# Optimization experiments

Measured on AMD Instinct MI355X. Metric: run time of the kernel, lower is better.

Reference implementation:

```python
import jax, jax.numpy as jnp
import numpy as np
from jax import lax

B, S, N, F = 64, 512, 30, 1
H, HD = 2, 8              # n_heads, head_dim (gat_hidden=16)
GH = H * HD               # gat_hidden
P = 64                    # projection_dim
LH = 64                   # lstm_hidden
ALPHA = 0.2


def setup_inputs() -> dict:
    key = jax.random.key(0)
    ks = jax.random.split(key, 16)
    x = jax.random.normal(ks[0], (B, S, N, F), dtype=jnp.float32)
    adj = jax.random.randint(ks[1], (N, N), 0, 2).astype(jnp.float32)
    adj = jnp.maximum(adj, jnp.eye(N, dtype=jnp.float32))  # self-loops, no empty rows
    sc = 0.1
    W_gat = sc * jax.random.normal(ks[2], (H, F, HD), dtype=jnp.float32)
    a_src = sc * jax.random.normal(ks[3], (H, HD), dtype=jnp.float32)
    a_dst = sc * jax.random.normal(ks[4], (H, HD), dtype=jnp.float32)
    W_proj = sc * jax.random.normal(ks[5], (N * GH, P), dtype=jnp.float32)
    b_proj = jnp.zeros((P,), dtype=jnp.float32)
    W_ih0 = sc * jax.random.normal(ks[6], (4 * LH, P), dtype=jnp.float32)
    W_hh0 = sc * jax.random.normal(ks[7], (4 * LH, LH), dtype=jnp.float32)
    b_ih0 = jnp.zeros((4 * LH,), dtype=jnp.float32)
    b_hh0 = jnp.zeros((4 * LH,), dtype=jnp.float32)
    W_ih1 = sc * jax.random.normal(ks[8], (4 * LH, LH), dtype=jnp.float32)
    W_hh1 = sc * jax.random.normal(ks[9], (4 * LH, LH), dtype=jnp.float32)
    b_ih1 = jnp.zeros((4 * LH,), dtype=jnp.float32)
    b_hh1 = jnp.zeros((4 * LH,), dtype=jnp.float32)
    W_out = sc * jax.random.normal(ks[10], (LH, N * F), dtype=jnp.float32)
    b_out = jnp.zeros((N * F,), dtype=jnp.float32)
    return dict(x=x, adj=adj, W_gat=W_gat, a_src=a_src, a_dst=a_dst,
                W_proj=W_proj, b_proj=b_proj,
                W_ih0=W_ih0, W_hh0=W_hh0, b_ih0=b_ih0, b_hh0=b_hh0,
                W_ih1=W_ih1, W_hh1=W_hh1, b_ih1=b_ih1, b_hh1=b_hh1,
                W_out=W_out, b_out=b_out)


def _gat(x_flat, adj, W_gat, a_src, a_dst):
    # x_flat: (BS, N, F)
    h = jnp.einsum('bnf,hfd->bhnd', x_flat, W_gat)          # (BS, H, N, HD)
    e_src = jnp.einsum('bhnd,hd->bhn', h, a_src)
    e_dst = jnp.einsum('bhnd,hd->bhn', h, a_dst)
    e = e_src[..., :, None] + e_dst[..., None, :]           # (BS, H, N, N)
    e = jnp.where(e >= 0, e, ALPHA * e)                     # leaky_relu
    e = jnp.where(adj == 0, -jnp.inf, e)
    attn = jax.nn.softmax(e, axis=-1)
    attn = jnp.nan_to_num(attn, nan=0.0)
    out = jnp.einsum('bhij,bhjd->bhid', attn, h)            # (BS, H, N, HD)
    out = jnp.swapaxes(out, 1, 2).reshape(out.shape[0], N, GH)  # head-concat
    out = jnp.where(out > 0, out, jnp.expm1(out))           # elu
    attn_avg = attn.mean(axis=1)                            # (BS, N, N)
    return out, attn_avg


def _lstm_layer(xs, W_ih, W_hh, b_ih, b_hh):
    # xs: (B, S, D) -> (B, S, LH); torch gate order i,f,g,o
    b = xs.shape[0]
    h0 = jnp.zeros((b, LH), xs.dtype)
    c0 = jnp.zeros((b, LH), xs.dtype)

    def step(carry, x_t):
        h, c = carry
        gates = x_t @ W_ih.T + b_ih + h @ W_hh.T + b_hh
        i, f, g, o = jnp.split(gates, 4, axis=-1)
        i, f, o = jax.nn.sigmoid(i), jax.nn.sigmoid(f), jax.nn.sigmoid(o)
        g = jnp.tanh(g)
        c = f * c + i * g
        h = o * jnp.tanh(c)
        return (h, c), h

    (_, _), hs = lax.scan(step, (h0, c0), jnp.swapaxes(xs, 0, 1))
    return jnp.swapaxes(hs, 0, 1)


def reference(x, adj, W_gat, a_src, a_dst, W_proj, b_proj,
              W_ih0, W_hh0, b_ih0, b_hh0, W_ih1, W_hh1, b_ih1, b_hh1,
              W_out, b_out):
    b, s, n, f = x.shape
    x_flat = x.reshape(b * s, n, f)
    gat_out, attn = _gat(x_flat, adj, W_gat, a_src, a_dst)   # (BS,N,GH),(BS,N,N)
    gat_seq = gat_out.reshape(b, s, n * GH)
    gat_seq = jax.nn.relu(gat_seq @ W_proj + b_proj)         # (B,S,P)
    h1 = _lstm_layer(gat_seq, W_ih0, W_hh0, b_ih0, b_hh0)
    h2 = _lstm_layer(h1, W_ih1, W_hh1, b_ih1, b_hh1)
    recon = h2 @ W_out + b_out                               # (B,S,N*F)
    attn_last = attn.reshape(b, s, n, n)[:, -1]              # (B,N,N)
    return recon, attn_last
```

## Files before the change

kernel.cpp:

```cpp
#include <hip/hip_runtime.h>
#include <math.h>

#define BS_TOT 32768
#define NN 30
#define HHD 8
#define GHH 16
#define LHH 64
#define SSS 512
#define BBB 64
#define RECON_SIZE (BBB*SSS*NN)

__device__ __forceinline__ float fsigmoid(float x) {
    return 1.f / (1.f + __expf(-x));
}
__device__ __forceinline__ float ftanh(float x) {
    float ax = fabsf(x);
    float e = __expf(-2.f * ax);
    float r = (1.f - e) / (1.f + e);
    return copysignf(r, x);
}

#define NB 16
__global__ __launch_bounds__(256) void gat_proj_kernel(
    const float* __restrict__ x, const float* __restrict__ adj,
    const float* __restrict__ W_gat, const float* __restrict__ a_src,
    const float* __restrict__ a_dst, const float* __restrict__ W_proj,
    const float* __restrict__ b_proj, float* __restrict__ gat_seq,
    float* __restrict__ attn_out)
{
    __shared__ __align__(16) float gat[NB][480];
    __shared__ __align__(16) float wchunk[96*64];
    __shared__ float x_s[NB][32];
    __shared__ unsigned adjbits[32];

    const int t = threadIdx.x;
    const int bs_base = blockIdx.x * NB;

    for (int rep = 0; rep < 2; ++rep) {
        int idx = rep*256 + t;
        int bl = idx >> 5, j = idx & 31;
        if (j < NN) x_s[bl][j] = x[(bs_base + bl)*NN + j];
    }
    if (t < NN) {
        unsigned bits = 0;
        for (int j = 0; j < NN; ++j)
            if (adj[t*NN + j] != 0.0f) bits |= (1u << j);
        adjbits[t] = bits;
    }
    __syncthreads();

    const int wave = t >> 6, lane = t & 63;
    const int h = lane >> 5, i = lane & 31;
    const bool act = (i < NN);

    float wg[HHD];
    float s_h = 0.f, t_h = 0.f;
    #pragma unroll
    for (int d = 0; d < HHD; ++d) {
        float w = W_gat[h*HHD + d];
        wg[d] = w;
        s_h += w * a_src[h*HHD + d];
        t_h += w * a_dst[h*HHD + d];
    }

    for (int r = 0; r < 4; ++r) {
        const int bl = wave*4 + r;
        const int bs = bs_base + bl;
        const unsigned bits = act ? adjbits[i & 31] : 0u;
        const float xi = act ? x_s[bl][i] : 0.f;
        const float esrc = xi * s_h;

        float m = -1e30f;
        for (int j = 0; j < NN; ++j) {
            if (bits & (1u << j)) {
                float e = esrc + x_s[bl][j] * t_h;
                e = (e >= 0.f) ? e : 0.2f * e;
                m = fmaxf(m, e);
            }
        }
        float Z = 0.f, Sx = 0.f;
        for (int j = 0; j < NN; ++j) {
            if (bits & (1u << j)) {
                float e = esrc + x_s[bl][j] * t_h;
                e = (e >= 0.f) ? e : 0.2f * e;
                float p = expf(e - m);
                Z += p;
                Sx += p * x_s[bl][j];
            }
        }
        const float wsum = Sx / Z;

        if (act) {
            float tmp[8];
            #pragma unroll
            for (int d = 0; d < 8; ++d) {
                float v = wsum * wg[d];
                tmp[d] = (v > 0.f) ? v : expm1f(v);
            }
            float4 v0 = make_float4(tmp[0], tmp[1], tmp[2], tmp[3]);
            float4 v1 = make_float4(tmp[4], tmp[5], tmp[6], tmp[7]);
            *(float4*)&gat[bl][i*GHH + h*HHD]     = v0;
            *(float4*)&gat[bl][i*GHH + h*HHD + 4] = v1;
        }

        if ((bs & (SSS-1)) == (SSS-1)) {
            const int b = bs >> 9;
            for (int j = 0; j < NN; ++j) {
                float a = 0.f;
                if (bits & (1u << j)) {
                    float e = esrc + x_s[bl][j] * t_h;
                    e = (e >= 0.f) ? e : 0.2f * e;
                    a = expf(e - m) / Z;
                }
                float ao = __shfl_xor(a, 32, 64);
                if (act && h == 0)
                    attn_out[b*(NN*NN) + i*NN + j] = 0.5f * (a + ao);
            }
        }
    }
    __syncthreads();

    const int p = t & 63, grp = t >> 6;
    float acc0 = 0.f, acc1 = 0.f, acc2 = 0.f, acc3 = 0.f;
    for (int c = 0; c < 5; ++c) {
        #pragma unroll
        for (int rep = 0; rep < 24; ++rep)
            wchunk[rep*256 + t] = W_proj[c*6144 + rep*256 + t];
        __syncthreads();
        for (int kk = 0; kk < 96; kk += 4) {
            float4 g0 = *(const float4*)&gat[grp*4 + 0][c*96 + kk];
            float4 g1 = *(const float4*)&gat[grp*4 + 1][c*96 + kk];
            float4 g2 = *(const float4*)&gat[grp*4 + 2][c*96 + kk];
            float4 g3 = *(const float4*)&gat[grp*4 + 3][c*96 + kk];
            float w0 = wchunk[(kk+0)*64 + p];
            float w1 = wchunk[(kk+1)*64 + p];
            float w2 = wchunk[(kk+2)*64 + p];
            float w3 = wchunk[(kk+3)*64 + p];
            acc0 += g0.x*w0 + g0.y*w1 + g0.z*w2 + g0.w*w3;
            acc1 += g1.x*w0 + g1.y*w1 + g1.z*w2 + g1.w*w3;
            acc2 += g2.x*w0 + g2.y*w1 + g2.z*w2 + g2.w*w3;
            acc3 += g3.x*w0 + g3.y*w1 + g3.z*w2 + g3.w*w3;
        }
        __syncthreads();
    }
    const float bp = b_proj[p];
    gat_seq[(bs_base + grp*4 + 0)*64 + p] = fmaxf(acc0 + bp, 0.f);
    gat_seq[(bs_base + grp*4 + 1)*64 + p] = fmaxf(acc1 + bp, 0.f);
    gat_seq[(bs_base + grp*4 + 2)*64 + p] = fmaxf(acc2 + bp, 0.f);
    gat_seq[(bs_base + grp*4 + 3)*64 + p] = fmaxf(acc3 + bp, 0.f);
}

__global__ __launch_bounds__(256) void xproj_kernel(
    const float* __restrict__ xin,
    const float* __restrict__ W,
    const float* __restrict__ b_ih, const float* __restrict__ b_hh,
    float* __restrict__ gx)
{
    __shared__ __align__(16) float xt[64][64];
    const int t = threadIdx.x;
    const int r0 = blockIdx.x * 64;

    for (int i = t; i < 64*16; i += 256) {
        int r = i >> 4, c4 = (i & 15) << 2;
        *(float4*)&xt[r][c4] = *(const float4*)&xin[(size_t)(r0 + r)*64 + c4];
    }
    float4 w[16];
    #pragma unroll
    for (int i = 0; i < 16; ++i) w[i] = *(const float4*)&W[t*64 + 4*i];
    const float bias = b_ih[t] + b_hh[t];
    __syncthreads();

    for (int r = 0; r < 64; ++r) {
        float a0 = 0.f, a1 = 0.f, a2 = 0.f, a3 = 0.f;
        #pragma unroll
        for (int i = 0; i < 16; ++i) {
            float4 v = *(const float4*)&xt[r][4*i];
            a0 = fmaf(v.x, w[i].x, a0); a1 = fmaf(v.y, w[i].y, a1);
            a2 = fmaf(v.z, w[i].z, a2); a3 = fmaf(v.w, w[i].w, a3);
        }
        gx[(size_t)(r0 + r)*256 + t] = bias + ((a0 + a1) + (a2 + a3));
    }
}

__global__ __launch_bounds__(256) void lstm_rec_kernel(
    const float* __restrict__ gx,
    const float* __restrict__ W_hh,
    float* __restrict__ h_out)
{
    __shared__ __align__(16) float whh[256][68];
    __shared__ float h_s[64];
    __shared__ float gates[256];

    const int t = threadIdx.x;
    const int b = blockIdx.x;

    for (int i = t; i < 256*16; i += 256) {
        int r = i >> 4, c4 = (i & 15) << 2;
        *(float4*)&whh[r][c4] = *(const float4*)&W_hh[r*64 + c4];
    }
    if (t < 64) h_s[t] = 0.f;
    __syncthreads();

    const float* __restrict__ gxb = gx + (size_t)b * SSS * 256;
    float* __restrict__ hrow = h_out + (size_t)b * SSS * 64;

    float c = 0.f;
    float gx_cur = gxb[t];
    const int sect = t >> 6;

    for (int tt = 0; tt < SSS; ++tt) {
        float gx_next = (tt + 1 < SSS) ? gxb[(size_t)(tt+1)*256 + t] : 0.f;

        float a0 = 0.f, a1 = 0.f, a2 = 0.f, a3 = 0.f;
        #pragma unroll
        for (int i = 0; i < 16; ++i) {
            float4 h4 = *(const float4*)&h_s[4*i];
            float4 w4 = *(const float4*)&whh[t][4*i];
            a0 = fmaf(h4.x, w4.x, a0); a1 = fmaf(h4.y, w4.y, a1);
            a2 = fmaf(h4.z, w4.z, a2); a3 = fmaf(h4.w, w4.w, a3);
        }
        const float acc = gx_cur + ((a0 + a1) + (a2 + a3));
        const float a = (sect == 2) ? ftanh(acc) : fsigmoid(acc);
        gates[t] = a;
        __syncthreads();

        if (t < 64) {
            float ig = gates[t], fg = gates[64+t], gg = gates[128+t], og = gates[192+t];
            c = fg*c + ig*gg;
            float hv = og * ftanh(c);
            h_s[t] = hv;
            hrow[(size_t)tt*64 + t] = hv;
        }
        gx_cur = gx_next;
        __syncthreads();
    }
}

__global__ __launch_bounds__(256) void recon_kernel(
    const float* __restrict__ h2, const float* __restrict__ W_out,
    const float* __restrict__ b_out, float* __restrict__ out)
{
    __shared__ __align__(16) float hl[8*64];
    const int t = threadIdx.x;
    const int bs_base = blockIdx.x * 8;

    hl[t]       = h2[(size_t)bs_base*64 + t];
    hl[256 + t] = h2[(size_t)bs_base*64 + 256 + t];
    __syncthreads();

    if (t < 240) {
        const int bl = t / 30;
        const int n  = t - bl*30;
        float acc = b_out[n];
        #pragma unroll
        for (int k = 0; k < 64; ++k)
            acc += hl[bl*64 + k] * W_out[k*NN + n];
        out[(size_t)(bs_base + bl)*NN + n] = acc;
    }
}

extern "C" void kernel_launch(void* const* d_in, const int* in_sizes, int n_in,
                              void* d_out, int out_size, void* d_ws, size_t ws_size,
                              hipStream_t stream)
{
    const float* x      = (const float*)d_in[0];
    const float* adj    = (const float*)d_in[1];
    const float* W_gat  = (const float*)d_in[2];
    const float* a_src  = (const float*)d_in[3];
    const float* a_dst  = (const float*)d_in[4];
    const float* W_proj = (const float*)d_in[5];
    const float* b_proj = (const float*)d_in[6];
    const float* W_ih0  = (const float*)d_in[7];
    const float* W_hh0  = (const float*)d_in[8];
    const float* b_ih0  = (const float*)d_in[9];
    const float* b_hh0  = (const float*)d_in[10];
    const float* W_ih1  = (const float*)d_in[11];
    const float* W_hh1  = (const float*)d_in[12];
    const float* b_ih1  = (const float*)d_in[13];
    const float* b_hh1  = (const float*)d_in[14];
    const float* W_out  = (const float*)d_in[15];
    const float* b_out  = (const float*)d_in[16];

    float* out = (float*)d_out;
    float* gat_seq = (float*)d_ws;
    float* h1  = gat_seq + (size_t)BS_TOT*64;
    float* h2  = h1 + (size_t)BS_TOT*64;
    float* gxb = h2 + (size_t)BS_TOT*64;

    hipLaunchKernelGGL(gat_proj_kernel, dim3(BS_TOT/NB), dim3(256), 0, stream,
                       x, adj, W_gat, a_src, a_dst, W_proj, b_proj,
                       gat_seq, out + RECON_SIZE);
    hipLaunchKernelGGL(xproj_kernel, dim3(BS_TOT/64), dim3(256), 0, stream,
                       gat_seq, W_ih0, b_ih0, b_hh0, gxb);
    hipLaunchKernelGGL(lstm_rec_kernel, dim3(BBB), dim3(256), 0, stream,
                       gxb, W_hh0, h1);
    hipLaunchKernelGGL(xproj_kernel, dim3(BS_TOT/64), dim3(256), 0, stream,
                       h1, W_ih1, b_ih1, b_hh1, gxb);
    hipLaunchKernelGGL(lstm_rec_kernel, dim3(BBB), dim3(256), 0, stream,
                       gxb, W_hh1, h2);
    hipLaunchKernelGGL(recon_kernel, dim3(BS_TOT/8), dim3(256), 0, stream,
                       h2, W_out, b_out, out);
}
```

Before: 909.6 us.

## Split LSTM recurrent dot products across 4 lanes with register-held weights

Result: faster. 773.3 us (-15.0%).

```diff
diff --git a/kernel.cpp b/kernel.cpp
--- a/kernel.cpp
+++ b/kernel.cpp
@@ -182,22 +182,24 @@
     }
 }
 
-__global__ __launch_bounds__(256) void lstm_rec_kernel(
+__global__ __launch_bounds__(1024, 1) void lstm_rec_kernel(
     const float* __restrict__ gx,
     const float* __restrict__ W_hh,
     float* __restrict__ h_out)
 {
-    __shared__ __align__(16) float whh[256][68];
     __shared__ float h_s[64];
     __shared__ float gates[256];
 
     const int t = threadIdx.x;
     const int b = blockIdx.x;
-
-    for (int i = t; i < 256*16; i += 256) {
-        int r = i >> 4, c4 = (i & 15) << 2;
-        *(float4*)&whh[r][c4] = *(const float4*)&W_hh[r*64 + c4];
-    }
+    const int row = t >> 2, slice = t & 3;
+    const int sect = row >> 6;
+
+    const float4 w0 = *(const float4*)&W_hh[row*64 + slice*16 + 0];
+    const float4 w1 = *(const float4*)&W_hh[row*64 + slice*16 + 4];
+    const float4 w2 = *(const float4*)&W_hh[row*64 + slice*16 + 8];
+    const float4 w3 = *(const float4*)&W_hh[row*64 + slice*16 + 12];
+
     if (t < 64) h_s[t] = 0.f;
     __syncthreads();
 
@@ -205,23 +207,28 @@
     float* __restrict__ hrow = h_out + (size_t)b * SSS * 64;
 
     float c = 0.f;
-    float gx_cur = gxb[t];
-    const int sect = t >> 6;
+    float gx_cur = gxb[row];
 
     for (int tt = 0; tt < SSS; ++tt) {
-        float gx_next = (tt + 1 < SSS) ? gxb[(size_t)(tt+1)*256 + t] : 0.f;
-
-        float a0 = 0.f, a1 = 0.f, a2 = 0.f, a3 = 0.f;
-        #pragma unroll
-        for (int i = 0; i < 16; ++i) {
-            float4 h4 = *(const float4*)&h_s[4*i];
-            float4 w4 = *(const float4*)&whh[t][4*i];
-            a0 = fmaf(h4.x, w4.x, a0); a1 = fmaf(h4.y, w4.y, a1);
-            a2 = fmaf(h4.z, w4.z, a2); a3 = fmaf(h4.w, w4.w, a3);
-        }
-        const float acc = gx_cur + ((a0 + a1) + (a2 + a3));
+        float gx_next = (tt + 1 < SSS) ? gxb[(size_t)(tt+1)*256 + row] : 0.f;
+
+        const float4 h0 = *(const float4*)&h_s[slice*16 + 0];
+        const float4 h1 = *(const float4*)&h_s[slice*16 + 4];
+        const float4 h2 = *(const float4*)&h_s[slice*16 + 8];
+        const float4 h3 = *(const float4*)&h_s[slice*16 + 12];
+
+        float a0 = h0.x*w0.x + h0.y*w0.y + h0.z*w0.z + h0.w*w0.w;
+        float a1 = h1.x*w1.x + h1.y*w1.y + h1.z*w1.z + h1.w*w1.w;
+        float a2 = h2.x*w2.x + h2.y*w2.y + h2.z*w2.z + h2.w*w2.w;
+        float a3 = h3.x*w3.x + h3.y*w3.y + h3.z*w3.z + h3.w*w3.w;
+        float acc = (a0 + a1) + (a2 + a3);
+
+        acc += __shfl_xor(acc, 1, 64);
+        acc += __shfl_xor(acc, 2, 64);
+        acc += gx_cur;
+
         const float a = (sect == 2) ? ftanh(acc) : fsigmoid(acc);
-        gates[t] = a;
+        if (slice == 0) gates[row] = a;
         __syncthreads();
 
         if (t < 64) {
@@ -292,11 +299,11 @@
                        gat_seq, out + RECON_SIZE);
     hipLaunchKernelGGL(xproj_kernel, dim3(BS_TOT/64), dim3(256), 0, stream,
                        gat_seq, W_ih0, b_ih0, b_hh0, gxb);
-    hipLaunchKernelGGL(lstm_rec_kernel, dim3(BBB), dim3(256), 0, stream,
+    hipLaunchKernelGGL(lstm_rec_kernel, dim3(BBB), dim3(1024), 0, stream,
                        gxb, W_hh0, h1);
     hipLaunchKernelGGL(xproj_kernel, dim3(BS_TOT/64), dim3(256), 0, stream,
                        h1, W_ih1, b_ih1, b_hh1, gxb);
-    hipLaunchKernelGGL(lstm_rec_kernel, dim3(BBB), dim3(256), 0, stream,
+    hipLaunchKernelGGL(lstm_rec_kernel, dim3(BBB), dim3(1024), 0, stream,
                        gxb, W_hh1, h2);
     hipLaunchKernelGGL(recon_kernel, dim3(BS_TOT/8), dim3(256), 0, stream,
                        h2, W_out, b_out, out);
```
